# Performance work log

Hardware: AMD Instinct MI355X
Metric: run time of the kernel (lower is better)

## Reference

```python
import jax, jax.numpy as jnp
import numpy as np

BIG_NEG = 1e10  # mask fill value used by the original wlsep


def setup_inputs() -> dict:
    key = jax.random.key(0)
    k1, k2 = jax.random.split(key)
    B, C = 4096, 128
    output = jax.random.normal(k1, (B, C), dtype=jnp.float32)
    target = jax.random.randint(k2, (B, C), 0, 2, dtype=jnp.int32)
    return {"output": output, "target": target}


def reference(output, target):
    x = output.astype(jnp.float32)          # [B, C] logits
    labels = target.astype(jnp.float32)     # [B, C] {0,1}

    # ---- bce: -mean over all elements of log(sig) if target!=0 else log(1-sig)
    # log(sigmoid(x)) = log_sigmoid(x); log(1 - sigmoid(x)) = log_sigmoid(-x)
    log_p = jax.nn.log_sigmoid(x)
    log_1mp = jax.nn.log_sigmoid(-x)
    bce_loss = -jnp.mean(jnp.where(labels == 0, log_1mp, log_p))

    # ---- wlsep ----
    # mask[b,i,j] = labels[b,j] > labels[b,i]  (j positive, i negative)
    mask = (labels[:, None, :] > labels[:, :, None]).astype(jnp.float32)  # [B,C,C]
    # diffs[b,i,j] = scores[b,i] - scores[b,j]
    diffs = x[:, :, None] - x[:, None, :]                                  # [B,C,C]
    masked = diffs - (1.0 - mask) * BIG_NEG
    # F.pad(pad=(0,0,0,1)) appends a zero row along dim=1, then logsumexp over dim=1
    B, C = x.shape
    padded = jnp.concatenate([masked, jnp.zeros((B, 1, C), dtype=masked.dtype)], axis=1)
    lse = jax.nn.logsumexp(padded, axis=1)  # [B, C]
    pos = labels > 0
    wlsep_loss = jnp.sum(jnp.where(pos, lse, 0.0)) / jnp.sum(pos)

    return bce_loss + wlsep_loss
```

## Files before the change

kernel.cpp:

```cpp
#include <hip/hip_runtime.h>
#include <math.h>


#define C_DIM 128

__device__ __forceinline__ float neg_log_sigmoid(float z) {
    return fmaxf(-z, 0.0f) + log1pf(__expf(-fabsf(z)));
}

__global__ __launch_bounds__(256) void bce_wlsep_rows(
        const float* __restrict__ x, const int* __restrict__ t,
        float4* __restrict__ partials, int B) {
    const int wave = threadIdx.x >> 6;
    const int row  = blockIdx.x * 4 + wave;
    const int lane = threadIdx.x & 63;

    float bce = 0.0f, wl = 0.0f, pos = 0.0f;
    if (row < B) {
        const float2 xv = ((const float2*)(x + (size_t)row * C_DIM))[lane];
        const int2   tv = ((const int2*)(t + (size_t)row * C_DIM))[lane];
        const float x0 = xv.x, x1 = xv.y;
        const int   t0 = tv.x, t1 = tv.y;

        bce = neg_log_sigmoid(t0 ? x0 : -x0) + neg_log_sigmoid(t1 ? x1 : -x1);

        float m = -INFINITY;
        if (t0 == 0) m = x0;
        if (t1 == 0) m = fmaxf(m, x1);
        #pragma unroll
        for (int off = 32; off; off >>= 1) m = fmaxf(m, __shfl_down(m, off, 64));
        m = __shfl(m, 0, 64);

        float T = 0.0f;
        if (t0 == 0) T += __expf(x0 - m);
        if (t1 == 0) T += __expf(x1 - m);
        #pragma unroll
        for (int off = 32; off; off >>= 1) T += __shfl_down(T, off, 64);
        T = __shfl(T, 0, 64);

        if (t0) {
            float a = m - x0;
            wl += (a > 0.0f) ? a + __logf(T + __expf(-a)) : log1pf(T * __expf(a));
            pos += 1.0f;
        }
        if (t1) {
            float a = m - x1;
            wl += (a > 0.0f) ? a + __logf(T + __expf(-a)) : log1pf(T * __expf(a));
            pos += 1.0f;
        }
    }

    #pragma unroll
    for (int off = 32; off; off >>= 1) {
        bce += __shfl_down(bce, off, 64);
        wl  += __shfl_down(wl,  off, 64);
        pos += __shfl_down(pos, off, 64);
    }

    __shared__ float s[3][4];
    if (lane == 0) { s[0][wave] = bce; s[1][wave] = wl; s[2][wave] = pos; }
    __syncthreads();
    if (threadIdx.x == 0) {
        float4 p;
        p.x = s[0][0] + s[0][1] + s[0][2] + s[0][3];
        p.y = s[1][0] + s[1][1] + s[1][2] + s[1][3];
        p.z = s[2][0] + s[2][1] + s[2][2] + s[2][3];
        p.w = 0.0f;
        partials[blockIdx.x] = p;
    }
}

__global__ __launch_bounds__(256) void bce_wlsep_reduce(
        const float4* __restrict__ partials, float* __restrict__ out,
        int nblocks, float inv_BC) {
    const int lane = threadIdx.x & 63;
    const int wave = threadIdx.x >> 6;

    float bce = 0.0f, wl = 0.0f, pos = 0.0f;
    for (int i = threadIdx.x; i < nblocks; i += 256) {
        float4 p = partials[i];
        bce += p.x; wl += p.y; pos += p.z;
    }
    #pragma unroll
    for (int off = 32; off; off >>= 1) {
        bce += __shfl_down(bce, off, 64);
        wl  += __shfl_down(wl,  off, 64);
        pos += __shfl_down(pos, off, 64);
    }
    __shared__ float s[3][4];
    if (lane == 0) { s[0][wave] = bce; s[1][wave] = wl; s[2][wave] = pos; }
    __syncthreads();
    if (threadIdx.x == 0) {
        float b = s[0][0] + s[0][1] + s[0][2] + s[0][3];
        float w = s[1][0] + s[1][1] + s[1][2] + s[1][3];
        float p = s[2][0] + s[2][1] + s[2][2] + s[2][3];
        out[0] = b * inv_BC + w / p;
    }
}

extern "C" void kernel_launch(void* const* d_in, const int* in_sizes, int n_in,
                              void* d_out, int out_size, void* d_ws, size_t ws_size,
                              hipStream_t stream) {
    const float* x = (const float*)d_in[0];
    const int*   t = (const int*)d_in[1];
    float* out = (float*)d_out;
    float4* partials = (float4*)d_ws;

    const int total = in_sizes[0];
    const int B = total / C_DIM;
    const int blocks = (B + 3) / 4;

    bce_wlsep_rows<<<blocks, 256, 0, stream>>>(x, t, partials, B);
    bce_wlsep_reduce<<<1, 256, 0, stream>>>(partials, out, blocks,
                                            1.0f / (float)total);
}
```

Measured before the change: 62.77 us.

## Fuse final reduction via last-block atomic counter and process 8 rows per wave

Merges the row kernel and the single-block reduce kernel into one launch: each block publishes its partial sums and bumps an atomic counter, and the last block to arrive does the final reduction. Each wave now handles 8 rows, with all loads issued up front, which cuts the block count and adds memory-level parallelism. Shuffle reductions switch to xor butterflies so the broadcast step is no longer needed. A memset of the counter replaces the second kernel launch, and the partial buffer is hard-sized to 512 blocks.

```diff
diff --git a/kernel.cpp b/kernel.cpp
--- a/kernel.cpp
+++ b/kernel.cpp
@@ -3,98 +3,112 @@
 
 
 #define C_DIM 128
+#define RPW   8
+#define TPB   256
 
 __device__ __forceinline__ float neg_log_sigmoid(float z) {
     return fmaxf(-z, 0.0f) + log1pf(__expf(-fabsf(z)));
 }
 
-__global__ __launch_bounds__(256) void bce_wlsep_rows(
+__global__ __launch_bounds__(TPB) void bce_wlsep_fused(
         const float* __restrict__ x, const int* __restrict__ t,
-        float4* __restrict__ partials, int B) {
+        float* __restrict__ part,
+        unsigned int* __restrict__ counter,
+        float* __restrict__ out, int B, int nblocks, float inv_BC) {
     const int wave = threadIdx.x >> 6;
-    const int row  = blockIdx.x * 4 + wave;
     const int lane = threadIdx.x & 63;
+    const int row0 = (blockIdx.x * 4 + wave) * RPW;
 
-    float bce = 0.0f, wl = 0.0f, pos = 0.0f;
-    if (row < B) {
-        const float2 xv = ((const float2*)(x + (size_t)row * C_DIM))[lane];
-        const int2   tv = ((const int2*)(t + (size_t)row * C_DIM))[lane];
-        const float x0 = xv.x, x1 = xv.y;
-        const int   t0 = tv.x, t1 = tv.y;
+    float2 xs[RPW]; int2 ts[RPW];
+    #pragma unroll
+    for (int k = 0; k < RPW; ++k) {
+        const int r = row0 + k;
+        if (r < B) {
+            xs[k] = ((const float2*)(x + (size_t)r * C_DIM))[lane];
+            ts[k] = ((const int2*)(t + (size_t)r * C_DIM))[lane];
+        } else {
+            xs[k] = make_float2(0.f, 0.f); ts[k] = make_int2(1, 1);
+        }
+    }
 
-        bce = neg_log_sigmoid(t0 ? x0 : -x0) + neg_log_sigmoid(t1 ? x1 : -x1);
+    float bce = 0.f, wl = 0.f, pos = 0.f;
+    #pragma unroll
+    for (int k = 0; k < RPW; ++k) {
+        if (row0 + k >= B) break;
+        const float x0 = xs[k].x, x1 = xs[k].y;
+        const int   t0 = ts[k].x,  t1 = ts[k].y;
+
+        bce += neg_log_sigmoid(t0 ? x0 : -x0) + neg_log_sigmoid(t1 ? x1 : -x1);
 
         float m = -INFINITY;
         if (t0 == 0) m = x0;
         if (t1 == 0) m = fmaxf(m, x1);
         #pragma unroll
-        for (int off = 32; off; off >>= 1) m = fmaxf(m, __shfl_down(m, off, 64));
-        m = __shfl(m, 0, 64);
+        for (int off = 32; off; off >>= 1) m = fmaxf(m, __shfl_xor(m, off, 64));
 
-        float T = 0.0f;
+        float T = 0.f;
         if (t0 == 0) T += __expf(x0 - m);
         if (t1 == 0) T += __expf(x1 - m);
         #pragma unroll
-        for (int off = 32; off; off >>= 1) T += __shfl_down(T, off, 64);
-        T = __shfl(T, 0, 64);
+        for (int off = 32; off; off >>= 1) T += __shfl_xor(T, off, 64);
 
         if (t0) {
             float a = m - x0;
-            wl += (a > 0.0f) ? a + __logf(T + __expf(-a)) : log1pf(T * __expf(a));
-            pos += 1.0f;
+            wl += (a > 0.f) ? a + __logf(T + __expf(-a)) : log1pf(T * __expf(a));
+            pos += 1.f;
         }
         if (t1) {
             float a = m - x1;
-            wl += (a > 0.0f) ? a + __logf(T + __expf(-a)) : log1pf(T * __expf(a));
-            pos += 1.0f;
+            wl += (a > 0.f) ? a + __logf(T + __expf(-a)) : log1pf(T * __expf(a));
+            pos += 1.f;
         }
     }
 
     #pragma unroll
     for (int off = 32; off; off >>= 1) {
-        bce += __shfl_down(bce, off, 64);
-        wl  += __shfl_down(wl,  off, 64);
-        pos += __shfl_down(pos, off, 64);
+        bce += __shfl_xor(bce, off, 64);
+        wl  += __shfl_xor(wl,  off, 64);
+        pos += __shfl_xor(pos, off, 64);
     }
 
     __shared__ float s[3][4];
-    if (lane == 0) { s[0][wave] = bce; s[1][wave] = wl; s[2][wave] = pos; }
-    __syncthreads();
-    if (threadIdx.x == 0) {
-        float4 p;
-        p.x = s[0][0] + s[0][1] + s[0][2] + s[0][3];
-        p.y = s[1][0] + s[1][1] + s[1][2] + s[1][3];
-        p.z = s[2][0] + s[2][1] + s[2][2] + s[2][3];
-        p.w = 0.0f;
-        partials[blockIdx.x] = p;
-    }
-}
-
-__global__ __launch_bounds__(256) void bce_wlsep_reduce(
-        const float4* __restrict__ partials, float* __restrict__ out,
-        int nblocks, float inv_BC) {
-    const int lane = threadIdx.x & 63;
-    const int wave = threadIdx.x >> 6;
-
-    float bce = 0.0f, wl = 0.0f, pos = 0.0f;
-    for (int i = threadIdx.x; i < nblocks; i += 256) {
-        float4 p = partials[i];
-        bce += p.x; wl += p.y; pos += p.z;
-    }
-    #pragma unroll
-    for (int off = 32; off; off >>= 1) {
-        bce += __shfl_down(bce, off, 64);
-        wl  += __shfl_down(wl,  off, 64);
-        pos += __shfl_down(pos, off, 64);
-    }
-    __shared__ float s[3][4];
+    __shared__ int is_last;
     if (lane == 0) { s[0][wave] = bce; s[1][wave] = wl; s[2][wave] = pos; }
     __syncthreads();
     if (threadIdx.x == 0) {
         float b = s[0][0] + s[0][1] + s[0][2] + s[0][3];
         float w = s[1][0] + s[1][1] + s[1][2] + s[1][3];
         float p = s[2][0] + s[2][1] + s[2][2] + s[2][3];
-        out[0] = b * inv_BC + w / p;
+        __hip_atomic_store(&part[0*512 + blockIdx.x], b, __ATOMIC_RELAXED, __HIP_MEMORY_SCOPE_AGENT);
+        __hip_atomic_store(&part[1*512 + blockIdx.x], w, __ATOMIC_RELAXED, __HIP_MEMORY_SCOPE_AGENT);
+        __hip_atomic_store(&part[2*512 + blockIdx.x], p, __ATOMIC_RELAXED, __HIP_MEMORY_SCOPE_AGENT);
+        unsigned old = __hip_atomic_fetch_add(counter, 1u, __ATOMIC_ACQ_REL, __HIP_MEMORY_SCOPE_AGENT);
+        is_last = (old == (unsigned)(nblocks - 1));
+    }
+    __syncthreads();
+
+    if (is_last) {
+        float b = 0.f, w = 0.f, p = 0.f;
+        for (int i = threadIdx.x; i < nblocks; i += TPB) {
+            b += __hip_atomic_load(&part[0*512 + i], __ATOMIC_RELAXED, __HIP_MEMORY_SCOPE_AGENT);
+            w += __hip_atomic_load(&part[1*512 + i], __ATOMIC_RELAXED, __HIP_MEMORY_SCOPE_AGENT);
+            p += __hip_atomic_load(&part[2*512 + i], __ATOMIC_RELAXED, __HIP_MEMORY_SCOPE_AGENT);
+        }
+        #pragma unroll
+        for (int off = 32; off; off >>= 1) {
+            b += __shfl_xor(b, off, 64);
+            w += __shfl_xor(w, off, 64);
+            p += __shfl_xor(p, off, 64);
+        }
+        __syncthreads();
+        if (lane == 0) { s[0][wave] = b; s[1][wave] = w; s[2][wave] = p; }
+        __syncthreads();
+        if (threadIdx.x == 0) {
+            float fb = s[0][0] + s[0][1] + s[0][2] + s[0][3];
+            float fw = s[1][0] + s[1][1] + s[1][2] + s[1][3];
+            float fp = s[2][0] + s[2][1] + s[2][2] + s[2][3];
+            out[0] = fb * inv_BC + fw / fp;
+        }
     }
 }
 
@@ -104,13 +118,15 @@
     const float* x = (const float*)d_in[0];
     const int*   t = (const int*)d_in[1];
     float* out = (float*)d_out;
-    float4* partials = (float4*)d_ws;
+
+    float* part = (float*)d_ws;
+    unsigned int* counter = (unsigned int*)((char*)d_ws + 3 * 512 * sizeof(float));
 
     const int total = in_sizes[0];
     const int B = total / C_DIM;
-    const int blocks = (B + 3) / 4;
+    const int blocks = (B + RPW * 4 - 1) / (RPW * 4);
 
-    bce_wlsep_rows<<<blocks, 256, 0, stream>>>(x, t, partials, B);
-    bce_wlsep_reduce<<<1, 256, 0, stream>>>(partials, out, blocks,
-                                            1.0f / (float)total);
+    hipMemsetAsync(counter, 0, sizeof(unsigned int), stream);
+    bce_wlsep_fused<<<blocks, TPB, 0, stream>>>(x, t, part, counter, out,
+                                                B, blocks, 1.0f / (float)total);
 }
```

After: 71.12 us. +13.3%, slower.
